# Optimization experiments

Measured on AMD Instinct MI355X. Metric: run time of the kernel, lower is better.

The kernel has to match this reference:

```python
import jax, jax.numpy as jnp
import numpy as np

N_NODES = 40000
N_EDGES = 640000
IN_CH = 128
OUT_CH = 128
NUM_RBF = 64


def setup_inputs() -> dict:
    key = jax.random.key(0)
    ks = jax.random.split(key, 8)
    x = jax.random.normal(ks[0], (N_NODES, IN_CH), dtype=jnp.float32)
    edge_index = jax.random.randint(ks[1], (2, N_EDGES), 0, N_NODES, dtype=jnp.int64)
    edge_rbf = jax.random.uniform(ks[2], (N_EDGES, NUM_RBF), dtype=jnp.float32)
    s1 = 1.0 / np.sqrt(NUM_RBF)
    s2 = 1.0 / np.sqrt(OUT_CH)
    sl = 1.0 / np.sqrt(IN_CH)
    W1 = jax.random.normal(ks[3], (NUM_RBF, OUT_CH), dtype=jnp.float32) * s1
    b1 = jnp.zeros((OUT_CH,), dtype=jnp.float32)
    W2 = jax.random.normal(ks[4], (OUT_CH, OUT_CH), dtype=jnp.float32) * s2
    b2 = jnp.zeros((OUT_CH,), dtype=jnp.float32)
    Wl = jax.random.normal(ks[5], (IN_CH, OUT_CH), dtype=jnp.float32) * sl
    bl = jnp.zeros((OUT_CH,), dtype=jnp.float32)
    return {"x": x, "edge_index": edge_index, "edge_rbf": edge_rbf,
            "W1": W1, "b1": b1, "W2": W2, "b2": b2, "Wl": Wl, "bl": bl}


def reference(x, edge_index, edge_rbf, W1, b1, W2, b2, Wl, bl):
    # filter_net: Linear -> ReLU -> Linear on edge RBF features  [E, OUT_CH]
    weight = jnp.maximum(edge_rbf @ W1 + b1, 0.0) @ W2 + b2
    # node linear projection  [N, OUT_CH]
    h = x @ Wl + bl
    row, col = edge_index[0], edge_index[1]
    # gather source node features, modulate by continuous filter
    msg = h[col] * weight  # [E, OUT_CH]
    # scatter-sum messages onto destination nodes
    out = jax.ops.segment_sum(msg, row, num_segments=x.shape[0])
    return out
```

## Files before the change

kernel.cpp:

```cpp
#include <hip/hip_runtime.h>


#define N_NODES 40000
#define N_EDGES 640000
#define IN_CH 128
#define OUT_CH 128
#define NUM_RBF 64

#define TILE_M 64
#define NTILES (N_EDGES / TILE_M)
#define NB_NODE (N_NODES / TILE_M)
#define RBF_STR 72
#define T_STR 136
#define HV_STR 136
#define W1_STR 72
#define W2_STR 136
#define NSCB ((N_NODES + 255) / 256)
#define EDGE_GRID 1024
#define K1_GRID 1024
#define ZC_BLOCKS 32

typedef __attribute__((ext_vector_type(8))) short bf16x8;
typedef __attribute__((ext_vector_type(16))) float f32x16;

__device__ __forceinline__ unsigned short f2bf(float f) {
  unsigned u = __float_as_uint(f);
  return (unsigned short)((u + 0x7FFFu + ((u >> 16) & 1u)) >> 16);
}
__device__ __forceinline__ float bf2f(unsigned short s) {
  return __uint_as_float(((unsigned)s) << 16);
}

__global__ __launch_bounds__(256) void k1_kernel(
    const float* __restrict__ x, const float* __restrict__ Wl,
    const float* __restrict__ bl, unsigned short* __restrict__ hbf,
    int* __restrict__ count, float* __restrict__ outp) {
  __shared__ __align__(16) char pool[IN_CH * W2_STR * 2];
  const int bid = blockIdx.x;
  const int t = threadIdx.x;

  if (bid >= NB_NODE) {
    if (bid < NB_NODE + ZC_BLOCKS) {
      if (count) {
        int4 z = {0, 0, 0, 0};
        for (int i = (bid - NB_NODE) * 256 + t; i < N_NODES / 4;
             i += ZC_BLOCKS * 256)
          ((int4*)count)[i] = z;
      }
    } else {
      if (outp) {
        float4 z = {0.f, 0.f, 0.f, 0.f};
        const int nb = K1_GRID - NB_NODE - ZC_BLOCKS;
        for (int i = (bid - NB_NODE - ZC_BLOCKS) * 256 + t;
             i < N_NODES * OUT_CH / 4; i += nb * 256)
          ((float4*)outp)[i] = z;
      }
    }
    return;
  }

  const int lane = t & 63;
  const int l31 = lane & 31;
  const int lhalf = lane >> 5;
  const int wv = t >> 6;
  const int nbase = wv * 32 + l31;

  {
    unsigned short* sWT = (unsigned short*)pool;
    const int k2 = t >> 1;
    const int d0 = (t & 1) * 64;
#pragma unroll
    for (int i = 0; i < 16; ++i) {
      float4 v = *(const float4*)(Wl + k2 * OUT_CH + d0 + 4 * i);
      sWT[(d0 + 4 * i + 0) * W2_STR + k2] = f2bf(v.x);
      sWT[(d0 + 4 * i + 1) * W2_STR + k2] = f2bf(v.y);
      sWT[(d0 + 4 * i + 2) * W2_STR + k2] = f2bf(v.z);
      sWT[(d0 + 4 * i + 3) * W2_STR + k2] = f2bf(v.w);
    }
  }
  __syncthreads();
  bf16x8 BW[8];
  {
    const unsigned short* sWT = (const unsigned short*)pool;
#pragma unroll
    for (int kk = 0; kk < 8; ++kk)
      BW[kk] = *(const bf16x8*)&sWT[nbase * W2_STR + kk * 16 + lhalf * 8];
  }
  const float blv = bl[nbase];
  __syncthreads();

  const int rbase = bid * TILE_M;
  unsigned short* sX = (unsigned short*)pool;
  {
    const int m = t >> 2;
    const int c0 = (t & 3) * 32;
    const float* src = x + (size_t)(rbase + m) * IN_CH + c0;
#pragma unroll
    for (int i = 0; i < 8; ++i) {
      float4 v = *(const float4*)(src + 4 * i);
      ushort4 p;
      p.x = f2bf(v.x); p.y = f2bf(v.y); p.z = f2bf(v.z); p.w = f2bf(v.w);
      *(ushort4*)&sX[m * T_STR + c0 + 4 * i] = p;
    }
  }
  __syncthreads();
#pragma unroll
  for (int mt = 0; mt < 2; ++mt) {
    f32x16 acc = {0.f, 0.f, 0.f, 0.f, 0.f, 0.f, 0.f, 0.f,
                  0.f, 0.f, 0.f, 0.f, 0.f, 0.f, 0.f, 0.f};
#pragma unroll
    for (int kk = 0; kk < 8; ++kk) {
      bf16x8 A = *(const bf16x8*)&sX[(mt * 32 + l31) * T_STR + kk * 16 + lhalf * 8];
      acc = __builtin_amdgcn_mfma_f32_32x32x16_bf16(A, BW[kk], acc, 0, 0, 0);
    }
#pragma unroll
    for (int r = 0; r < 16; ++r) {
      const int rowm = mt * 32 + (r & 3) + 8 * (r >> 2) + 4 * lhalf;
      hbf[(size_t)(rbase + rowm) * OUT_CH + nbase] = f2bf(acc[r] + blv);
    }
  }
}

__global__ void hist_kernel(const int* __restrict__ rowI, int* __restrict__ count,
                            unsigned long long* __restrict__ status) {
  if (blockIdx.x == 0 && threadIdx.x < NSCB) status[threadIdx.x] = 0ULL;
  int e = blockIdx.x * 256 + threadIdx.x;
  if (e < N_EDGES) atomicAdd(&count[rowI[e]], 1);
}

__global__ __launch_bounds__(256) void scan_kernel(
    const int* __restrict__ count, unsigned long long* __restrict__ status,
    int* __restrict__ cursor) {
  __shared__ int s[256];
  __shared__ int wsum[4];
  const int t = threadIdx.x;
  const int b = blockIdx.x;
  const int i = b * 256 + t;
  const int v = (i < N_NODES) ? count[i] : 0;
  s[t] = v;
  __syncthreads();
  for (int off = 1; off < 256; off <<= 1) {
    int u = (t >= off) ? s[t - off] : 0;
    __syncthreads();
    s[t] += u;
    __syncthreads();
  }
  if (t == 255)
    __hip_atomic_store(&status[b], (1ULL << 32) | (unsigned)s[255],
                       __ATOMIC_RELEASE, __HIP_MEMORY_SCOPE_AGENT);
  int contrib = 0;
  if (t < b) {
    unsigned long long sv;
    do {
      sv = __hip_atomic_load(&status[t], __ATOMIC_ACQUIRE,
                             __HIP_MEMORY_SCOPE_AGENT);
    } while (!(sv >> 32));
    contrib = (int)(unsigned)sv;
  }
  for (int o = 32; o > 0; o >>= 1) contrib += __shfl_down(contrib, o, 64);
  if ((t & 63) == 0) wsum[t >> 6] = contrib;
  __syncthreads();
  const int boffv = wsum[0] + wsum[1] + wsum[2] + wsum[3];
  if (i < N_NODES) cursor[i] = boffv + s[t] - v;
}

__global__ void scatter_kernel(const int* __restrict__ rowI,
                               const int* __restrict__ colI,
                               int* __restrict__ cursor,
                               unsigned long long* __restrict__ packed) {
  int e = blockIdx.x * 256 + threadIdx.x;
  if (e < N_EDGES) {
    const int r = rowI[e];
    const int c = colI[e];
    const int p = atomicAdd(&cursor[r], 1);
    packed[p] = ((unsigned long long)r << 36) | ((unsigned long long)c << 20) |
                (unsigned)e;
  }
}

__global__ __launch_bounds__(256, 4) void edge_fused_kernel(
    const unsigned long long* __restrict__ packed, const float* __restrict__ rbf,
    const float* __restrict__ W1, const float* __restrict__ b1,
    const float* __restrict__ W2, const float* __restrict__ b2,
    const unsigned short* __restrict__ hbf, float* __restrict__ outp) {
  __shared__ __align__(16) char pool[IN_CH * W2_STR * 2];

  unsigned short* sHv = (unsigned short*)pool;
  unsigned short* sT = (unsigned short*)pool;
  unsigned short* sRbf = (unsigned short*)(pool + TILE_M * HV_STR * 2);
  int* sAux = (int*)(pool + TILE_M * HV_STR * 2 + TILE_M * RBF_STR * 2);

  const int t = threadIdx.x;
  const int lane = t & 63;
  const int l31 = lane & 31;
  const int lhalf = lane >> 5;
  const int wv = t >> 6;
  const int nbase = wv * 32 + l31;

  {
    unsigned short* sW1T = (unsigned short*)pool;
    const int k = t >> 2;
    const int c0 = (t & 3) * 32;
#pragma unroll
    for (int i = 0; i < 8; ++i) {
      float4 v = *(const float4*)(W1 + k * OUT_CH + c0 + 4 * i);
      sW1T[(c0 + 4 * i + 0) * W1_STR + k] = f2bf(v.x);
      sW1T[(c0 + 4 * i + 1) * W1_STR + k] = f2bf(v.y);
      sW1T[(c0 + 4 * i + 2) * W1_STR + k] = f2bf(v.z);
      sW1T[(c0 + 4 * i + 3) * W1_STR + k] = f2bf(v.w);
    }
  }
  __syncthreads();
  bf16x8 B1[4];
  {
    const unsigned short* sW1T = (const unsigned short*)pool;
#pragma unroll
    for (int kk = 0; kk < 4; ++kk)
      B1[kk] = *(const bf16x8*)&sW1T[nbase * W1_STR + kk * 16 + lhalf * 8];
  }
  __syncthreads();
  {
    unsigned short* sW2T = (unsigned short*)pool;
    const int k2 = t >> 1;
    const int d0 = (t & 1) * 64;
#pragma unroll
    for (int i = 0; i < 16; ++i) {
      float4 v = *(const float4*)(W2 + k2 * OUT_CH + d0 + 4 * i);
      sW2T[(d0 + 4 * i + 0) * W2_STR + k2] = f2bf(v.x);
      sW2T[(d0 + 4 * i + 1) * W2_STR + k2] = f2bf(v.y);
      sW2T[(d0 + 4 * i + 2) * W2_STR + k2] = f2bf(v.z);
      sW2T[(d0 + 4 * i + 3) * W2_STR + k2] = f2bf(v.w);
    }
  }
  __syncthreads();
  bf16x8 B2[8];
  {
    const unsigned short* sW2T = (const unsigned short*)pool;
#pragma unroll
    for (int kk = 0; kk < 8; ++kk)
      B2[kk] = *(const bf16x8*)&sW2T[nbase * W2_STR + kk * 16 + lhalf * 8];
  }
  const float b1v = b1[nbase];
  const float b2v = b2[nbase];

  const int m4 = t >> 2;
  const int kq = (t & 3) * 16;

  float4 rbfreg[4];
  uint4 hvreg[4];
  int auxv = 0;

  auto prefetch = [&](int tl) {
    const int eb = tl * TILE_M;
    const unsigned long long pkm = packed[eb + m4];
    const float* src = rbf + (size_t)(pkm & 0xFFFFFu) * NUM_RBF + kq;
#pragma unroll
    for (int i = 0; i < 4; ++i) rbfreg[i] = *(const float4*)(src + 4 * i);
#pragma unroll
    for (int i = 0; i < 4; ++i) {
      const int chunk = t + 256 * i;
      const int row = chunk >> 4;
      const int c8 = (chunk & 15) * 8;
      const unsigned long long pkr = packed[eb + row];
      const int col = (int)((pkr >> 20) & 0xFFFFu);
      hvreg[i] = *(const uint4*)(hbf + (size_t)col * OUT_CH + c8);
    }
    if (t < TILE_M) auxv = (int)(packed[eb + t] >> 36);
  };

  int tile = blockIdx.x;
  if (tile < NTILES) prefetch(tile);

  for (; tile < NTILES; tile += gridDim.x) {
    __syncthreads();

#pragma unroll
    for (int i = 0; i < 4; ++i) {
      float4 v = rbfreg[i];
      ushort4 p;
      p.x = f2bf(v.x); p.y = f2bf(v.y); p.z = f2bf(v.z); p.w = f2bf(v.w);
      *(ushort4*)&sRbf[m4 * RBF_STR + kq + 4 * i] = p;
    }
#pragma unroll
    for (int i = 0; i < 4; ++i) {
      const int chunk = t + 256 * i;
      const int row = chunk >> 4;
      const int c8 = (chunk & 15) * 8;
      *(uint4*)&sHv[row * HV_STR + c8] = hvreg[i];
    }
    if (t < TILE_M) sAux[t] = auxv;
    __syncthreads();

    const int tn = tile + gridDim.x;
    if (tn < NTILES) prefetch(tn);

    float hv[2][16];
#pragma unroll
    for (int mt = 0; mt < 2; ++mt)
#pragma unroll
      for (int r = 0; r < 16; ++r) {
        const int rowm = mt * 32 + (r & 3) + 8 * (r >> 2) + 4 * lhalf;
        hv[mt][r] = bf2f(sHv[rowm * HV_STR + nbase]);
      }
    __syncthreads();

#pragma unroll
    for (int mt = 0; mt < 2; ++mt) {
      f32x16 acc = {0.f, 0.f, 0.f, 0.f, 0.f, 0.f, 0.f, 0.f,
                    0.f, 0.f, 0.f, 0.f, 0.f, 0.f, 0.f, 0.f};
#pragma unroll
      for (int kk = 0; kk < 4; ++kk) {
        bf16x8 A = *(const bf16x8*)&sRbf[(mt * 32 + l31) * RBF_STR + kk * 16 + lhalf * 8];
        acc = __builtin_amdgcn_mfma_f32_32x32x16_bf16(A, B1[kk], acc, 0, 0, 0);
      }
#pragma unroll
      for (int r = 0; r < 16; ++r) {
        const int rowm = (r & 3) + 8 * (r >> 2) + 4 * lhalf;
        float v = acc[r] + b1v;
        v = v > 0.f ? v : 0.f;
        sT[(mt * 32 + rowm) * T_STR + nbase] = f2bf(v);
      }
    }
    __syncthreads();

    float sum = 0.f;
    int curd = -1;
#pragma unroll
    for (int mt = 0; mt < 2; ++mt) {
      f32x16 acc = {0.f, 0.f, 0.f, 0.f, 0.f, 0.f, 0.f, 0.f,
                    0.f, 0.f, 0.f, 0.f, 0.f, 0.f, 0.f, 0.f};
#pragma unroll
      for (int kk = 0; kk < 8; ++kk) {
        bf16x8 A = *(const bf16x8*)&sT[(mt * 32 + l31) * T_STR + kk * 16 + lhalf * 8];
        acc = __builtin_amdgcn_mfma_f32_32x32x16_bf16(A, B2[kk], acc, 0, 0, 0);
      }
#pragma unroll
      for (int r = 0; r < 16; ++r) {
        const int rowm = mt * 32 + (r & 3) + 8 * (r >> 2) + 4 * lhalf;
        const float m = hv[mt][r] * (acc[r] + b2v);
        const int d = sAux[rowm];
        if (d != curd) {
          if (curd >= 0) atomicAdd(&outp[(size_t)curd * OUT_CH + nbase], sum);
          curd = d;
          sum = m;
        } else {
          sum += m;
        }
      }
    }
    atomicAdd(&outp[(size_t)curd * OUT_CH + nbase], sum);
  }
}

__global__ __launch_bounds__(256, 4) void edge_atomic_kernel(
    const int* __restrict__ eidx, const float* __restrict__ rbf,
    const float* __restrict__ W1, const float* __restrict__ b1,
    const float* __restrict__ W2, const float* __restrict__ b2,
    const unsigned short* __restrict__ hbf, float* __restrict__ outp) {
  __shared__ __align__(16) char pool[IN_CH * W2_STR * 2];

  unsigned short* sHv = (unsigned short*)pool;
  unsigned short* sT = (unsigned short*)pool;
  unsigned short* sRbf = (unsigned short*)(pool + TILE_M * HV_STR * 2);
  int* sAux = (int*)(pool + TILE_M * HV_STR * 2 + TILE_M * RBF_STR * 2);

  const int t = threadIdx.x;
  const int lane = t & 63;
  const int l31 = lane & 31;
  const int lhalf = lane >> 5;
  const int wv = t >> 6;
  const int nbase = wv * 32 + l31;

  {
    unsigned short* sW1T = (unsigned short*)pool;
    const int k = t >> 2;
    const int c0 = (t & 3) * 32;
#pragma unroll
    for (int i = 0; i < 8; ++i) {
      float4 v = *(const float4*)(W1 + k * OUT_CH + c0 + 4 * i);
      sW1T[(c0 + 4 * i + 0) * W1_STR + k] = f2bf(v.x);
      sW1T[(c0 + 4 * i + 1) * W1_STR + k] = f2bf(v.y);
      sW1T[(c0 + 4 * i + 2) * W1_STR + k] = f2bf(v.z);
      sW1T[(c0 + 4 * i + 3) * W1_STR + k] = f2bf(v.w);
    }
  }
  __syncthreads();
  bf16x8 B1[4];
  {
    const unsigned short* sW1T = (const unsigned short*)pool;
#pragma unroll
    for (int kk = 0; kk < 4; ++kk)
      B1[kk] = *(const bf16x8*)&sW1T[nbase * W1_STR + kk * 16 + lhalf * 8];
  }
  __syncthreads();
  {
    unsigned short* sW2T = (unsigned short*)pool;
    const int k2 = t >> 1;
    const int d0 = (t & 1) * 64;
#pragma unroll
    for (int i = 0; i < 16; ++i) {
      float4 v = *(const float4*)(W2 + k2 * OUT_CH + d0 + 4 * i);
      sW2T[(d0 + 4 * i + 0) * W2_STR + k2] = f2bf(v.x);
      sW2T[(d0 + 4 * i + 1) * W2_STR + k2] = f2bf(v.y);
      sW2T[(d0 + 4 * i + 2) * W2_STR + k2] = f2bf(v.z);
      sW2T[(d0 + 4 * i + 3) * W2_STR + k2] = f2bf(v.w);
    }
  }
  __syncthreads();
  bf16x8 B2[8];
  {
    const unsigned short* sW2T = (const unsigned short*)pool;
#pragma unroll
    for (int kk = 0; kk < 8; ++kk)
      B2[kk] = *(const bf16x8*)&sW2T[nbase * W2_STR + kk * 16 + lhalf * 8];
  }
  const float b1v = b1[nbase];
  const float b2v = b2[nbase];

  const int* rowI = eidx;
  const int* colI = eidx + N_EDGES;

  for (int tile = blockIdx.x; tile < NTILES; tile += gridDim.x) {
    const int ebase = tile * TILE_M;
    __syncthreads();
    {
      const int m = t >> 2;
      const int kq = (t & 3) * 16;
      const float* src = rbf + (size_t)(ebase + m) * NUM_RBF + kq;
#pragma unroll
      for (int i = 0; i < 4; ++i) {
        float4 v = *(const float4*)(src + 4 * i);
        ushort4 p;
        p.x = f2bf(v.x); p.y = f2bf(v.y); p.z = f2bf(v.z); p.w = f2bf(v.w);
        *(ushort4*)&sRbf[m * RBF_STR + kq + 4 * i] = p;
      }
#pragma unroll
      for (int i = 0; i < 4; ++i) {
        const int chunk = t + 256 * i;
        const int row = chunk >> 4;
        const int c8 = (chunk & 15) * 8;
        const int col = colI[ebase + row];
        *(uint4*)&sHv[row * HV_STR + c8] =
            *(const uint4*)(hbf + (size_t)col * OUT_CH + c8);
      }
      if (t < TILE_M) sAux[t] = rowI[ebase + t];
    }
    __syncthreads();

    float hv[2][16];
#pragma unroll
    for (int mt = 0; mt < 2; ++mt)
#pragma unroll
      for (int r = 0; r < 16; ++r) {
        const int rowm = mt * 32 + (r & 3) + 8 * (r >> 2) + 4 * lhalf;
        hv[mt][r] = bf2f(sHv[rowm * HV_STR + nbase]);
      }
    __syncthreads();

#pragma unroll
    for (int mt = 0; mt < 2; ++mt) {
      f32x16 acc = {0.f, 0.f, 0.f, 0.f, 0.f, 0.f, 0.f, 0.f,
                    0.f, 0.f, 0.f, 0.f, 0.f, 0.f, 0.f, 0.f};
#pragma unroll
      for (int kk = 0; kk < 4; ++kk) {
        bf16x8 A = *(const bf16x8*)&sRbf[(mt * 32 + l31) * RBF_STR + kk * 16 + lhalf * 8];
        acc = __builtin_amdgcn_mfma_f32_32x32x16_bf16(A, B1[kk], acc, 0, 0, 0);
      }
#pragma unroll
      for (int r = 0; r < 16; ++r) {
        const int rowm = (r & 3) + 8 * (r >> 2) + 4 * lhalf;
        float v = acc[r] + b1v;
        v = v > 0.f ? v : 0.f;
        sT[(mt * 32 + rowm) * T_STR + nbase] = f2bf(v);
      }
    }
    __syncthreads();

    float sum = 0.f;
    int curd = -1;
#pragma unroll
    for (int mt = 0; mt < 2; ++mt) {
      f32x16 acc = {0.f, 0.f, 0.f, 0.f, 0.f, 0.f, 0.f, 0.f,
                    0.f, 0.f, 0.f, 0.f, 0.f, 0.f, 0.f, 0.f};
#pragma unroll
      for (int kk = 0; kk < 8; ++kk) {
        bf16x8 A = *(const bf16x8*)&sT[(mt * 32 + l31) * T_STR + kk * 16 + lhalf * 8];
        acc = __builtin_amdgcn_mfma_f32_32x32x16_bf16(A, B2[kk], acc, 0, 0, 0);
      }
#pragma unroll
      for (int r = 0; r < 16; ++r) {
        const int rowm = mt * 32 + (r & 3) + 8 * (r >> 2) + 4 * lhalf;
        const float m = hv[mt][r] * (acc[r] + b2v);
        const int d = sAux[rowm];
        if (d != curd) {
          if (curd >= 0) atomicAdd(&outp[(size_t)curd * OUT_CH + nbase], sum);
          curd = d;
          sum = m;
        } else {
          sum += m;
        }
      }
    }
    atomicAdd(&outp[(size_t)curd * OUT_CH + nbase], sum);
  }
}

extern "C" void kernel_launch(void* const* d_in, const int* in_sizes, int n_in,
                              void* d_out, int out_size, void* d_ws, size_t ws_size,
                              hipStream_t stream) {
  const float* x    = (const float*)d_in[0];
  const int*   eidx = (const int*)d_in[1];
  const float* rbf  = (const float*)d_in[2];
  const float* W1   = (const float*)d_in[3];
  const float* b1   = (const float*)d_in[4];
  const float* W2   = (const float*)d_in[5];
  const float* b2   = (const float*)d_in[6];
  const float* Wl   = (const float*)d_in[7];
  const float* bl   = (const float*)d_in[8];
  float* out = (float*)d_out;

  char* ws = (char*)d_ws;
  const size_t HBF_B = (size_t)N_NODES * OUT_CH * 2;
  const size_t PK_B = (size_t)N_EDGES * 8;
  const size_t CNT_B = (size_t)N_NODES * 4;
  const size_t ST_B = 1280;
  const size_t need = HBF_B + PK_B + 2 * CNT_B + ST_B + 64;

  size_t off = 0;
  unsigned short* hbf = (unsigned short*)(ws + off); off += HBF_B;
  unsigned long long* packed = (unsigned long long*)(ws + off); off += PK_B;
  int* count  = (int*)(ws + off); off += CNT_B;
  int* cursor = (int*)(ws + off); off += CNT_B;
  unsigned long long* status = (unsigned long long*)(ws + off); off += ST_B;

  const int* rowI = eidx;
  const int* colI = eidx + N_EDGES;

  if (ws_size >= need) {
    k1_kernel<<<K1_GRID, 256, 0, stream>>>(x, Wl, bl, hbf, count, out);
    hist_kernel<<<(N_EDGES + 255) / 256, 256, 0, stream>>>(rowI, count, status);
    scan_kernel<<<NSCB, 256, 0, stream>>>(count, status, cursor);
    scatter_kernel<<<(N_EDGES + 255) / 256, 256, 0, stream>>>(
        rowI, colI, cursor, packed);
    edge_fused_kernel<<<EDGE_GRID, 256, 0, stream>>>(
        packed, rbf, W1, b1, W2, b2, hbf, out);
  } else {
    hipMemsetAsync(out, 0, (size_t)N_NODES * OUT_CH * sizeof(float), stream);
    k1_kernel<<<NB_NODE, 256, 0, stream>>>(x, Wl, bl, hbf, nullptr, nullptr);
    edge_atomic_kernel<<<EDGE_GRID, 256, 0, stream>>>(
        eidx, rbf, W1, b1, W2, b2, hbf, out);
  }
}
```

Baseline: 496.6 us.

## Shrink edge-kernel LDS pool, raise occupancy to five blocks, drop register prefetch

The weight transpose staging now loads W2 in two 64-row halves through a 72-stride buffer, so the shared pool shrinks to about 26.9 KB. Launch bounds go from four to five blocks per CU and the edge grid from 1024 to 1280 blocks. The register double-buffer prefetch of rbf and h tiles is replaced by direct loads into LDS each iteration. This frees registers and LDS for the higher occupancy, but gives up the explicit overlap of the next tile's gathers with the current tile's compute.

```diff
diff --git a/kernel.cpp b/kernel.cpp
--- a/kernel.cpp
+++ b/kernel.cpp
@@ -13,12 +13,13 @@
 #define RBF_STR 72
 #define T_STR 136
 #define HV_STR 136
-#define W1_STR 72
+#define W_STR 72
 #define W2_STR 136
 #define NSCB ((N_NODES + 255) / 256)
-#define EDGE_GRID 1024
+#define EDGE_GRID 1280
 #define K1_GRID 1024
 #define ZC_BLOCKS 32
+#define POOL_B 26880
 
 typedef __attribute__((ext_vector_type(8))) short bf16x8;
 typedef __attribute__((ext_vector_type(16))) float f32x16;
@@ -178,12 +179,12 @@
   }
 }
 
-__global__ __launch_bounds__(256, 4) void edge_fused_kernel(
+__global__ __launch_bounds__(256, 5) void edge_fused_kernel(
     const unsigned long long* __restrict__ packed, const float* __restrict__ rbf,
     const float* __restrict__ W1, const float* __restrict__ b1,
     const float* __restrict__ W2, const float* __restrict__ b2,
     const unsigned short* __restrict__ hbf, float* __restrict__ outp) {
-  __shared__ __align__(16) char pool[IN_CH * W2_STR * 2];
+  __shared__ __align__(16) char pool[POOL_B];
 
   unsigned short* sHv = (unsigned short*)pool;
   unsigned short* sT = (unsigned short*)pool;
@@ -197,48 +198,51 @@
   const int wv = t >> 6;
   const int nbase = wv * 32 + l31;
 
-  {
-    unsigned short* sW1T = (unsigned short*)pool;
-    const int k = t >> 2;
-    const int c0 = (t & 3) * 32;
-#pragma unroll
-    for (int i = 0; i < 8; ++i) {
-      float4 v = *(const float4*)(W1 + k * OUT_CH + c0 + 4 * i);
-      sW1T[(c0 + 4 * i + 0) * W1_STR + k] = f2bf(v.x);
-      sW1T[(c0 + 4 * i + 1) * W1_STR + k] = f2bf(v.y);
-      sW1T[(c0 + 4 * i + 2) * W1_STR + k] = f2bf(v.z);
-      sW1T[(c0 + 4 * i + 3) * W1_STR + k] = f2bf(v.w);
-    }
-  }
-  __syncthreads();
+  unsigned short* sWT = (unsigned short*)pool;
+  const int kst = t >> 2;
+  const int dst0 = (t & 3) * 32;
+
   bf16x8 B1[4];
-  {
-    const unsigned short* sW1T = (const unsigned short*)pool;
-#pragma unroll
-    for (int kk = 0; kk < 4; ++kk)
-      B1[kk] = *(const bf16x8*)&sW1T[nbase * W1_STR + kk * 16 + lhalf * 8];
-  }
-  __syncthreads();
-  {
-    unsigned short* sW2T = (unsigned short*)pool;
-    const int k2 = t >> 1;
-    const int d0 = (t & 1) * 64;
-#pragma unroll
-    for (int i = 0; i < 16; ++i) {
-      float4 v = *(const float4*)(W2 + k2 * OUT_CH + d0 + 4 * i);
-      sW2T[(d0 + 4 * i + 0) * W2_STR + k2] = f2bf(v.x);
-      sW2T[(d0 + 4 * i + 1) * W2_STR + k2] = f2bf(v.y);
-      sW2T[(d0 + 4 * i + 2) * W2_STR + k2] = f2bf(v.z);
-      sW2T[(d0 + 4 * i + 3) * W2_STR + k2] = f2bf(v.w);
-    }
-  }
-  __syncthreads();
   bf16x8 B2[8];
   {
-    const unsigned short* sW2T = (const unsigned short*)pool;
-#pragma unroll
-    for (int kk = 0; kk < 8; ++kk)
-      B2[kk] = *(const bf16x8*)&sW2T[nbase * W2_STR + kk * 16 + lhalf * 8];
+#pragma unroll
+    for (int i = 0; i < 8; ++i) {
+      float4 v = *(const float4*)(W1 + kst * OUT_CH + dst0 + 4 * i);
+      sWT[(dst0 + 4 * i + 0) * W_STR + kst] = f2bf(v.x);
+      sWT[(dst0 + 4 * i + 1) * W_STR + kst] = f2bf(v.y);
+      sWT[(dst0 + 4 * i + 2) * W_STR + kst] = f2bf(v.z);
+      sWT[(dst0 + 4 * i + 3) * W_STR + kst] = f2bf(v.w);
+    }
+    __syncthreads();
+#pragma unroll
+    for (int kk = 0; kk < 4; ++kk)
+      B1[kk] = *(const bf16x8*)&sWT[nbase * W_STR + kk * 16 + lhalf * 8];
+    __syncthreads();
+#pragma unroll
+    for (int i = 0; i < 8; ++i) {
+      float4 v = *(const float4*)(W2 + kst * OUT_CH + dst0 + 4 * i);
+      sWT[(dst0 + 4 * i + 0) * W_STR + kst] = f2bf(v.x);
+      sWT[(dst0 + 4 * i + 1) * W_STR + kst] = f2bf(v.y);
+      sWT[(dst0 + 4 * i + 2) * W_STR + kst] = f2bf(v.z);
+      sWT[(dst0 + 4 * i + 3) * W_STR + kst] = f2bf(v.w);
+    }
+    __syncthreads();
+#pragma unroll
+    for (int kk = 0; kk < 4; ++kk)
+      B2[kk] = *(const bf16x8*)&sWT[nbase * W_STR + kk * 16 + lhalf * 8];
+    __syncthreads();
+#pragma unroll
+    for (int i = 0; i < 8; ++i) {
+      float4 v = *(const float4*)(W2 + (64 + kst) * OUT_CH + dst0 + 4 * i);
+      sWT[(dst0 + 4 * i + 0) * W_STR + kst] = f2bf(v.x);
+      sWT[(dst0 + 4 * i + 1) * W_STR + kst] = f2bf(v.y);
+      sWT[(dst0 + 4 * i + 2) * W_STR + kst] = f2bf(v.z);
+      sWT[(dst0 + 4 * i + 3) * W_STR + kst] = f2bf(v.w);
+    }
+    __syncthreads();
+#pragma unroll
+    for (int kk = 0; kk < 4; ++kk)
+      B2[4 + kk] = *(const bf16x8*)&sWT[nbase * W_STR + kk * 16 + lhalf * 8];
   }
   const float b1v = b1[nbase];
   const float b2v = b2[nbase];
@@ -246,53 +250,32 @@
   const int m4 = t >> 2;
   const int kq = (t & 3) * 16;
 
-  float4 rbfreg[4];
-  uint4 hvreg[4];
-  int auxv = 0;
-
-  auto prefetch = [&](int tl) {
-    const int eb = tl * TILE_M;
-    const unsigned long long pkm = packed[eb + m4];
-    const float* src = rbf + (size_t)(pkm & 0xFFFFFu) * NUM_RBF + kq;
-#pragma unroll
-    for (int i = 0; i < 4; ++i) rbfreg[i] = *(const float4*)(src + 4 * i);
-#pragma unroll
-    for (int i = 0; i < 4; ++i) {
-      const int chunk = t + 256 * i;
-      const int row = chunk >> 4;
-      const int c8 = (chunk & 15) * 8;
-      const unsigned long long pkr = packed[eb + row];
-      const int col = (int)((pkr >> 20) & 0xFFFFu);
-      hvreg[i] = *(const uint4*)(hbf + (size_t)col * OUT_CH + c8);
-    }
-    if (t < TILE_M) auxv = (int)(packed[eb + t] >> 36);
-  };
-
-  int tile = blockIdx.x;
-  if (tile < NTILES) prefetch(tile);
-
-  for (; tile < NTILES; tile += gridDim.x) {
-    __syncthreads();
-
-#pragma unroll
-    for (int i = 0; i < 4; ++i) {
-      float4 v = rbfreg[i];
-      ushort4 p;
-      p.x = f2bf(v.x); p.y = f2bf(v.y); p.z = f2bf(v.z); p.w = f2bf(v.w);
-      *(ushort4*)&sRbf[m4 * RBF_STR + kq + 4 * i] = p;
-    }
-#pragma unroll
-    for (int i = 0; i < 4; ++i) {
-      const int chunk = t + 256 * i;
-      const int row = chunk >> 4;
-      const int c8 = (chunk & 15) * 8;
-      *(uint4*)&sHv[row * HV_STR + c8] = hvreg[i];
-    }
-    if (t < TILE_M) sAux[t] = auxv;
-    __syncthreads();
-
-    const int tn = tile + gridDim.x;
-    if (tn < NTILES) prefetch(tn);
+  for (int tile = blockIdx.x; tile < NTILES; tile += gridDim.x) {
+    const int ebase = tile * TILE_M;
+    __syncthreads();
+
+    {
+      const unsigned long long pkm = packed[ebase + m4];
+      const float* src = rbf + (size_t)(pkm & 0xFFFFFu) * NUM_RBF + kq;
+#pragma unroll
+      for (int i = 0; i < 4; ++i) {
+        float4 v = *(const float4*)(src + 4 * i);
+        ushort4 p;
+        p.x = f2bf(v.x); p.y = f2bf(v.y); p.z = f2bf(v.z); p.w = f2bf(v.w);
+        *(ushort4*)&sRbf[m4 * RBF_STR + kq + 4 * i] = p;
+      }
+#pragma unroll
+      for (int i = 0; i < 4; ++i) {
+        const int chunk = t + 256 * i;
+        const int row = chunk >> 4;
+        const int c8 = (chunk & 15) * 8;
+        const int col = (int)((packed[ebase + row] >> 20) & 0xFFFFu);
+        *(uint4*)&sHv[row * HV_STR + c8] =
+            *(const uint4*)(hbf + (size_t)col * OUT_CH + c8);
+      }
+      if (t < TILE_M) sAux[t] = (int)(packed[ebase + t] >> 36);
+    }
+    __syncthreads();
 
     float hv[2][16];
 #pragma unroll
@@ -352,12 +335,12 @@
   }
 }
 
-__global__ __launch_bounds__(256, 4) void edge_atomic_kernel(
+__global__ __launch_bounds__(256, 5) void edge_atomic_kernel(
     const int* __restrict__ eidx, const float* __restrict__ rbf,
     const float* __restrict__ W1, const float* __restrict__ b1,
     const float* __restrict__ W2, const float* __restrict__ b2,
     const unsigned short* __restrict__ hbf, float* __restrict__ outp) {
-  __shared__ __align__(16) char pool[IN_CH * W2_STR * 2];
+  __shared__ __align__(16) char pool[POOL_B];
 
   unsigned short* sHv = (unsigned short*)pool;
   unsigned short* sT = (unsigned short*)pool;
@@ -371,48 +354,51 @@
   const int wv = t >> 6;
   const int nbase = wv * 32 + l31;
 
-  {
-    unsigned short* sW1T = (unsigned short*)pool;
-    const int k = t >> 2;
-    const int c0 = (t & 3) * 32;
-#pragma unroll
-    for (int i = 0; i < 8; ++i) {
-      float4 v = *(const float4*)(W1 + k * OUT_CH + c0 + 4 * i);
-      sW1T[(c0 + 4 * i + 0) * W1_STR + k] = f2bf(v.x);
-      sW1T[(c0 + 4 * i + 1) * W1_STR + k] = f2bf(v.y);
-      sW1T[(c0 + 4 * i + 2) * W1_STR + k] = f2bf(v.z);
-      sW1T[(c0 + 4 * i + 3) * W1_STR + k] = f2bf(v.w);
-    }
-  }
-  __syncthreads();
+  unsigned short* sWT = (unsigned short*)pool;
+  const int kst = t >> 2;
+  const int dst0 = (t & 3) * 32;
+
   bf16x8 B1[4];
-  {
-    const unsigned short* sW1T = (const unsigned short*)pool;
-#pragma unroll
-    for (int kk = 0; kk < 4; ++kk)
-      B1[kk] = *(const bf16x8*)&sW1T[nbase * W1_STR + kk * 16 + lhalf * 8];
-  }
-  __syncthreads();
-  {
-    unsigned short* sW2T = (unsigned short*)pool;
-    const int k2 = t >> 1;
-    const int d0 = (t & 1) * 64;
-#pragma unroll
-    for (int i = 0; i < 16; ++i) {
-      float4 v = *(const float4*)(W2 + k2 * OUT_CH + d0 + 4 * i);
-      sW2T[(d0 + 4 * i + 0) * W2_STR + k2] = f2bf(v.x);
-      sW2T[(d0 + 4 * i + 1) * W2_STR + k2] = f2bf(v.y);
-      sW2T[(d0 + 4 * i + 2) * W2_STR + k2] = f2bf(v.z);
-      sW2T[(d0 + 4 * i + 3) * W2_STR + k2] = f2bf(v.w);
-    }
-  }
-  __syncthreads();
   bf16x8 B2[8];
   {
-    const unsigned short* sW2T = (const unsigned short*)pool;
-#pragma unroll
-    for (int kk = 0; kk < 8; ++kk)
-      B2[kk] = *(const bf16x8*)&sW2T[nbase * W2_STR + kk * 16 + lhalf * 8];
+#pragma unroll
+    for (int i = 0; i < 8; ++i) {
+      float4 v = *(const float4*)(W1 + kst * OUT_CH + dst0 + 4 * i);
+      sWT[(dst0 + 4 * i + 0) * W_STR + kst] = f2bf(v.x);
+      sWT[(dst0 + 4 * i + 1) * W_STR + kst] = f2bf(v.y);
+      sWT[(dst0 + 4 * i + 2) * W_STR + kst] = f2bf(v.z);
+      sWT[(dst0 + 4 * i + 3) * W_STR + kst] = f2bf(v.w);
+    }
+    __syncthreads();
+#pragma unroll
+    for (int kk = 0; kk < 4; ++kk)
+      B1[kk] = *(const bf16x8*)&sWT[nbase * W_STR + kk * 16 + lhalf * 8];
+    __syncthreads();
+#pragma unroll
+    for (int i = 0; i < 8; ++i) {
+      float4 v = *(const float4*)(W2 + kst * OUT_CH + dst0 + 4 * i);
+      sWT[(dst0 + 4 * i + 0) * W_STR + kst] = f2bf(v.x);
+      sWT[(dst0 + 4 * i + 1) * W_STR + kst] = f2bf(v.y);
+      sWT[(dst0 + 4 * i + 2) * W_STR + kst] = f2bf(v.z);
+      sWT[(dst0 + 4 * i + 3) * W_STR + kst] = f2bf(v.w);
+    }
+    __syncthreads();
+#pragma unroll
+    for (int kk = 0; kk < 4; ++kk)
+      B2[kk] = *(const bf16x8*)&sWT[nbase * W_STR + kk * 16 + lhalf * 8];
+    __syncthreads();
+#pragma unroll
+    for (int i = 0; i < 8; ++i) {
+      float4 v = *(const float4*)(W2 + (64 + kst) * OUT_CH + dst0 + 4 * i);
+      sWT[(dst0 + 4 * i + 0) * W_STR + kst] = f2bf(v.x);
+      sWT[(dst0 + 4 * i + 1) * W_STR + kst] = f2bf(v.y);
+      sWT[(dst0 + 4 * i + 2) * W_STR + kst] = f2bf(v.z);
+      sWT[(dst0 + 4 * i + 3) * W_STR + kst] = f2bf(v.w);
+    }
+    __syncthreads();
+#pragma unroll
+    for (int kk = 0; kk < 4; ++kk)
+      B2[4 + kk] = *(const bf16x8*)&sWT[nbase * W_STR + kk * 16 + lhalf * 8];
   }
   const float b1v = b1[nbase];
   const float b2v = b2[nbase];
```

Result: no change. 496.8 us (+0.0%).
